# Performance work log

Measured on AMD Instinct MI355X. Metric: run time of the kernel, lower is better.

The kernel has to match this reference:

```python
import jax, jax.numpy as jnp
import numpy as np

N_NODES = 100000
T = 1024        # number of visits / hyperedges (GRU sequence length)
IN = 128        # in_channel
HID = 256       # hid_channel


def setup_inputs() -> dict:
    key = jax.random.key(0)
    ks = jax.random.split(key, 7)
    X = jax.random.normal(ks[0], (N_NODES, IN), dtype=jnp.float32)
    H = jax.random.uniform(ks[1], (N_NODES, T), dtype=jnp.float32)
    s = 1.0 / np.sqrt(HID)  # torch default GRU init scale
    w_ih = jax.random.uniform(ks[2], (3 * HID, IN), jnp.float32, -s, s)
    w_hh = jax.random.uniform(ks[3], (3 * HID, HID), jnp.float32, -s, s)
    b_ih = jax.random.uniform(ks[4], (3 * HID,), jnp.float32, -s, s)
    b_hh = jax.random.uniform(ks[5], (3 * HID,), jnp.float32, -s, s)
    w_attn = jax.random.uniform(ks[6], (HID,), jnp.float32, -s, s)
    return {"X": X, "H": H, "w_ih": w_ih, "w_hh": w_hh,
            "b_ih": b_ih, "b_hh": b_hh, "w_attn": w_attn}


def _gru(visit_emb, w_ih, w_hh, b_ih, b_hh):
    # Precompute input-side gates for all timesteps: [T, 3H]
    gx = visit_emb @ w_ih.T + b_ih

    def step(h, gx_t):
        gh = h @ w_hh.T + b_hh
        xr, xz, xn = jnp.split(gx_t, 3)
        hr, hz, hn = jnp.split(gh, 3)
        r = jax.nn.sigmoid(xr + hr)
        z = jax.nn.sigmoid(xz + hz)
        n = jnp.tanh(xn + r * hn)
        h_new = (1.0 - z) * n + z * h
        return h_new, h_new

    h0 = jnp.zeros((HID,), visit_emb.dtype)
    _, hs = jax.lax.scan(step, h0, gx)
    return hs  # [T, HID]


def reference(X, H, w_ih, w_hh, b_ih, b_hh, w_attn):
    # visit_emb = H.T @ X : [T, IN]
    visit_emb = H.T @ X
    hs = _gru(visit_emb, w_ih, w_hh, b_ih, b_hh)          # [T, HID]
    alpha = jax.nn.softmax(hs @ w_attn)                    # [T]
    # sum(diag(alpha) @ hs, 0) == alpha-weighted sum of hidden states
    return alpha @ hs                                      # [HID]
```

## Files before the change

### kernel.cpp

```cpp
#include <hip/hip_runtime.h>
#include <hip/hip_fp16.h>

typedef _Float16 half8 __attribute__((ext_vector_type(8)));
typedef _Float16 half2v __attribute__((ext_vector_type(2)));
typedef float f32x4 __attribute__((ext_vector_type(4)));

#define T_STEPS 1024
#define INC 128
#define HIDC 256
#define G3 768
#define NN 100000
#define KSPLIT 32
#define NCHUNK 3125
#define XS_STRIDE 144

__device__ __forceinline__ float dpp_xor1(float v){
  int t = __builtin_amdgcn_update_dpp(0, __float_as_int(v), 0xB1, 0xF, 0xF, true);
  return __int_as_float(t);
}

__global__ __launch_bounds__(512) void k_phase1(const float* __restrict__ X,
                                                const float* __restrict__ Hm,
                                                float* __restrict__ part){
  const int bid = blockIdx.x;
  const int xcd = bid & 7;
  const int idx = bid >> 3;
  const int ks  = xcd * 4 + (idx & 3);
  const int tt  = idx >> 2;
  const int t0 = tt * 128;
  const int nbeg = ks * NCHUNK;
  const int nend = nbeg + NCHUNK;
  __shared__ float Hs[16][128];
  __shared__ float Xs[16 * XS_STRIDE];
  const int tid = threadIdx.x;
  const int tx = tid & 15;
  const int ty = tid >> 4;
  const int sr = tid >> 5;
  const int sc = tid & 31;
  const int xskew = tx * 8 + (tx >> 2) * 4;

  float acc[4][8];
  #pragma unroll
  for (int r = 0; r < 4; r++)
    #pragma unroll
    for (int q = 0; q < 8; q++) acc[r][q] = 0.f;

  float4 hv = make_float4(0.f,0.f,0.f,0.f), xv = make_float4(0.f,0.f,0.f,0.f);
  {
    int n = nbeg + sr;
    if (n < nend){
      hv = *(const float4*)(Hm + (size_t)n * T_STEPS + t0 + sc * 4);
      xv = *(const float4*)(X  + (size_t)n * INC + sc * 4);
    }
  }

  for (int n0 = nbeg; n0 < nend; n0 += 16){
    __builtin_amdgcn_s_barrier();
    asm volatile("" ::: "memory");
    *(float4*)&Hs[sr][sc * 4] = hv;
    {
      int g = sc >> 1, hf = sc & 1;
      *(float4*)&Xs[sr * XS_STRIDE + g * 8 + (g >> 2) * 4 + hf * 4] = xv;
    }
    asm volatile("s_waitcnt lgkmcnt(0)" ::: "memory");
    __builtin_amdgcn_s_barrier();
    asm volatile("" ::: "memory");

    {
      int nn = n0 + 16 + sr;
      hv = make_float4(0.f,0.f,0.f,0.f);
      xv = make_float4(0.f,0.f,0.f,0.f);
      if (nn < nend){
        hv = *(const float4*)(Hm + (size_t)nn * T_STEPS + t0 + sc * 4);
        xv = *(const float4*)(X  + (size_t)nn * INC + sc * 4);
      }
    }

    #pragma unroll
    for (int i = 0; i < 16; i++){
      float4 h4 = *(const float4*)&Hs[i][ty * 4];
      float4 x0 = *(const float4*)&Xs[i * XS_STRIDE + xskew];
      float4 x1 = *(const float4*)&Xs[i * XS_STRIDE + xskew + 4];
      float xr[8] = {x0.x,x0.y,x0.z,x0.w,x1.x,x1.y,x1.z,x1.w};
      float hr[4] = {h4.x,h4.y,h4.z,h4.w};
      #pragma unroll
      for (int r = 0; r < 4; r++)
        #pragma unroll
        for (int q = 0; q < 8; q++)
          acc[r][q] += hr[r] * xr[q];
    }
  }
  #pragma unroll
  for (int r = 0; r < 4; r++){
    size_t o = ((size_t)ks * T_STEPS + t0 + ty * 4 + r) * INC + tx * 8;
    *(float4*)&part[o]     = make_float4(acc[r][0], acc[r][1], acc[r][2], acc[r][3]);
    *(float4*)&part[o + 4] = make_float4(acc[r][4], acc[r][5], acc[r][6], acc[r][7]);
  }
}

__global__ __launch_bounds__(256) void k_reduce(const float* __restrict__ part,
                                                float* __restrict__ ve){
  int idx = blockIdx.x * 256 + threadIdx.x;
  float s = 0.f;
  #pragma unroll
  for (int ks = 0; ks < KSPLIT; ks++) s += part[(size_t)ks * (T_STEPS * INC) + idx];
  ve[idx] = s;
}

__global__ __launch_bounds__(768) void k_gx(const float* __restrict__ ve,
                                            const float* __restrict__ w_ih,
                                            const float* __restrict__ b_ih,
                                            const float* __restrict__ b_hh,
                                            float* __restrict__ gxq){
  const int t = blockIdx.x;
  const int j = threadIdx.x;
  __shared__ float4 v4[32];
  if (j < 32) v4[j] = *(const float4*)(ve + (size_t)t * INC + j * 4);
  __syncthreads();
  const float4* wr = (const float4*)(w_ih + (size_t)j * INC);
  float a0 = 0.f, a1 = 0.f, a2 = 0.f, a3 = 0.f;
  #pragma unroll
  for (int q = 0; q < 32; q++){
    float4 w = wr[q]; float4 v = v4[q];
    a0 += w.x * v.x; a1 += w.y * v.y; a2 += w.z * v.z; a3 += w.w * v.w;
  }
  float bias = b_ih[j] + (j < 512 ? b_hh[j] : 0.f);
  gxq[(size_t)t * 1024 + (j & 255) * 4 + (j >> 8)] = (a0 + a1) + (a2 + a3) + bias;
}

__global__ __launch_bounds__(512, 2) void k_gru(const float* __restrict__ w_hh,
                                                const float* __restrict__ b_hh,
                                                const float* __restrict__ gxq,
                                                float* __restrict__ hs){
  const int tid  = threadIdx.x;
  const int unit = tid >> 1;
  const int ks   = tid & 1;
  const int k0   = ks * 128;

  __shared__ _Float16 hbuf[2][256];

  half2v Bp[3][64];
  #pragma unroll
  for (int g = 0; g < 3; g++){
    const float* wr = w_hh + (size_t)(g * 256 + unit) * HIDC + k0;
    #pragma unroll
    for (int c = 0; c < 32; c++){
      float4 v = *(const float4*)(wr + c * 4);
      half2v p0; p0[0] = (_Float16)v.x; p0[1] = (_Float16)v.y;
      half2v p1; p1[0] = (_Float16)v.z; p1[1] = (_Float16)v.w;
      Bp[g][2 * c]     = p0;
      Bp[g][2 * c + 1] = p1;
    }
  }
  const float bn = b_hh[512 + unit];
  float hprev = 0.f;
  if (tid < 256) hbuf[0][tid] = (_Float16)0.f;
  __syncthreads();

  f32x4 gq = *(const f32x4*)(gxq + (size_t)unit * 4);

  for (int t = 0; t < T_STEPS; t++){
    const _Float16* hb = &hbuf[t & 1][k0];
    float ar0 = 0.f, ar1 = 0.f, az0 = 0.f, az1 = 0.f, an0 = 0.f, an1 = 0.f;
    #pragma unroll
    for (int c = 0; c < 16; c++){
      half8 hv = *(const half8*)(hb + c * 8);
      #pragma unroll
      for (int q = 0; q < 4; q++){
        half2v hp; hp[0] = hv[2 * q]; hp[1] = hv[2 * q + 1];
        if (c & 1){
          ar1 = __builtin_amdgcn_fdot2(hp, Bp[0][4 * c + q], ar1, false);
          az1 = __builtin_amdgcn_fdot2(hp, Bp[1][4 * c + q], az1, false);
          an1 = __builtin_amdgcn_fdot2(hp, Bp[2][4 * c + q], an1, false);
        } else {
          ar0 = __builtin_amdgcn_fdot2(hp, Bp[0][4 * c + q], ar0, false);
          az0 = __builtin_amdgcn_fdot2(hp, Bp[1][4 * c + q], az0, false);
          an0 = __builtin_amdgcn_fdot2(hp, Bp[2][4 * c + q], an0, false);
        }
      }
    }
    f32x4 gq_n = *(const f32x4*)(gxq + (size_t)(t + 1) * 1024 + unit * 4);

    float dr = ar0 + ar1; dr += dpp_xor1(dr);
    float dz = az0 + az1; dz += dpp_xor1(dz);
    float dn = an0 + an1; dn += dpp_xor1(dn);

    float r = 1.f / (1.f + __expf(-(gq[0] + dr)));
    float z = 1.f / (1.f + __expf(-(gq[1] + dz)));
    float pre = gq[2] + r * (dn + bn);
    float ax = fabsf(pre);
    float e = __expf(-2.f * ax);
    float th = (1.f - e) / (1.f + e);
    float n = copysignf(th, pre);
    float hnew = n + z * (hprev - n);
    hprev = hnew;
    if (ks == 0){
      hbuf[(t + 1) & 1][unit] = (_Float16)hnew;
      hs[(size_t)t * HIDC + unit] = hnew;
    }
    gq = gq_n;
    __syncthreads();
  }
}

__global__ __launch_bounds__(64) void k_logits(const float* __restrict__ hs,
                                               const float* __restrict__ w_attn,
                                               float* __restrict__ logits){
  int t = blockIdx.x;
  int l = threadIdx.x;
  float4 hv = *(const float4*)(hs + (size_t)t * HIDC + l * 4);
  float4 wv = *(const float4*)(w_attn + l * 4);
  float p = hv.x * wv.x + hv.y * wv.y + hv.z * wv.z + hv.w * wv.w;
  #pragma unroll
  for (int o = 32; o > 0; o >>= 1) p += __shfl_down(p, o);
  if (l == 0) logits[t] = p;
}

__global__ __launch_bounds__(1024) void k_attn(const float* __restrict__ logits,
                                               const float* __restrict__ hs,
                                               float* __restrict__ out){
  __shared__ float sm[1024];
  __shared__ float al[1024];
  __shared__ float ps[4][HIDC];
  int tid = threadIdx.x;
  float lg = logits[tid];
  sm[tid] = lg; __syncthreads();
  for (int s = 512; s > 0; s >>= 1){
    if (tid < s) sm[tid] = fmaxf(sm[tid], sm[tid + s]);
    __syncthreads();
  }
  float mx = sm[0]; __syncthreads();
  float e = __expf(lg - mx);
  sm[tid] = e; __syncthreads();
  for (int s = 512; s > 0; s >>= 1){
    if (tid < s) sm[tid] += sm[tid + s];
    __syncthreads();
  }
  float inv = 1.f / sm[0];
  al[tid] = e * inv;
  __syncthreads();
  int c = tid & 255; int tq = tid >> 8;
  float acc = 0.f;
  for (int t = tq; t < T_STEPS; t += 4) acc += al[t] * hs[(size_t)t * HIDC + c];
  ps[tq][c] = acc; __syncthreads();
  if (tid < HIDC) out[tid] = (ps[0][tid] + ps[1][tid]) + (ps[2][tid] + ps[3][tid]);
}

extern "C" void kernel_launch(void* const* d_in, const int* in_sizes, int n_in,
                              void* d_out, int out_size, void* d_ws, size_t ws_size,
                              hipStream_t stream){
  const float* X      = (const float*)d_in[0];
  const float* Hm     = (const float*)d_in[1];
  const float* w_ih   = (const float*)d_in[2];
  const float* w_hh   = (const float*)d_in[3];
  const float* b_ih   = (const float*)d_in[4];
  const float* b_hh   = (const float*)d_in[5];
  const float* w_attn = (const float*)d_in[6];
  float* out = (float*)d_out;

  float* ws     = (float*)d_ws;
  float* part   = ws;
  float* ve     = part + 4194304;
  float* gxq    = ve + 131072;
  float* hs     = gxq + 1049600;
  float* logits = hs + 262144;

  k_phase1<<<256, 512, 0, stream>>>(X, Hm, part);
  k_reduce<<<512, 256, 0, stream>>>(part, ve);
  k_gx<<<1024, 768, 0, stream>>>(ve, w_ih, b_ih, b_hh, gxq);
  k_gru<<<1, 512, 0, stream>>>(w_hh, b_hh, gxq, hs);
  k_logits<<<1024, 64, 0, stream>>>(hs, w_attn, logits);
  k_attn<<<1, 1024, 0, stream>>>(logits, hs, out);
}
```

Before: 2.196 ms.

## Split GRU recurrent matvec four ways per unit across 1024 threads

```diff
diff --git a/kernel.cpp b/kernel.cpp
--- a/kernel.cpp
+++ b/kernel.cpp
@@ -16,6 +16,10 @@
 
 __device__ __forceinline__ float dpp_xor1(float v){
   int t = __builtin_amdgcn_update_dpp(0, __float_as_int(v), 0xB1, 0xF, 0xF, true);
+  return __int_as_float(t);
+}
+__device__ __forceinline__ float dpp_xor2(float v){
+  int t = __builtin_amdgcn_update_dpp(0, __float_as_int(v), 0x4E, 0xF, 0xF, true);
   return __int_as_float(t);
 }
 
@@ -128,23 +132,23 @@
   gxq[(size_t)t * 1024 + (j & 255) * 4 + (j >> 8)] = (a0 + a1) + (a2 + a3) + bias;
 }
 
-__global__ __launch_bounds__(512, 2) void k_gru(const float* __restrict__ w_hh,
-                                                const float* __restrict__ b_hh,
-                                                const float* __restrict__ gxq,
-                                                float* __restrict__ hs){
+__global__ __launch_bounds__(1024) void k_gru(const float* __restrict__ w_hh,
+                                              const float* __restrict__ b_hh,
+                                              const float* __restrict__ gxq,
+                                              float* __restrict__ hs){
   const int tid  = threadIdx.x;
-  const int unit = tid >> 1;
-  const int ks   = tid & 1;
-  const int k0   = ks * 128;
+  const int unit = tid >> 2;
+  const int ks   = tid & 3;
+  const int k0   = ks * 64;
 
   __shared__ _Float16 hbuf[2][256];
 
-  half2v Bp[3][64];
+  half2v Bp[3][32];
   #pragma unroll
   for (int g = 0; g < 3; g++){
     const float* wr = w_hh + (size_t)(g * 256 + unit) * HIDC + k0;
     #pragma unroll
-    for (int c = 0; c < 32; c++){
+    for (int c = 0; c < 16; c++){
       float4 v = *(const float4*)(wr + c * 4);
       half2v p0; p0[0] = (_Float16)v.x; p0[1] = (_Float16)v.y;
       half2v p1; p1[0] = (_Float16)v.z; p1[1] = (_Float16)v.w;
@@ -157,33 +161,34 @@
   if (tid < 256) hbuf[0][tid] = (_Float16)0.f;
   __syncthreads();
 
-  f32x4 gq = *(const f32x4*)(gxq + (size_t)unit * 4);
-
   for (int t = 0; t < T_STEPS; t++){
     const _Float16* hb = &hbuf[t & 1][k0];
+    f32x4 gq = *(const f32x4*)(gxq + (size_t)t * 1024 + unit * 4);
+
     float ar0 = 0.f, ar1 = 0.f, az0 = 0.f, az1 = 0.f, an0 = 0.f, an1 = 0.f;
     #pragma unroll
-    for (int c = 0; c < 16; c++){
-      half8 hv = *(const half8*)(hb + c * 8);
+    for (int c = 0; c < 8; c++){
+      const int cc = (c + 2 * ks) & 7;
+      half8 hv = *(const half8*)(hb + cc * 8);
       #pragma unroll
       for (int q = 0; q < 4; q++){
         half2v hp; hp[0] = hv[2 * q]; hp[1] = hv[2 * q + 1];
+        const int j = cc * 4 + q;
         if (c & 1){
-          ar1 = __builtin_amdgcn_fdot2(hp, Bp[0][4 * c + q], ar1, false);
-          az1 = __builtin_amdgcn_fdot2(hp, Bp[1][4 * c + q], az1, false);
-          an1 = __builtin_amdgcn_fdot2(hp, Bp[2][4 * c + q], an1, false);
+          ar1 = __builtin_amdgcn_fdot2(hp, Bp[0][j], ar1, false);
+          az1 = __builtin_amdgcn_fdot2(hp, Bp[1][j], az1, false);
+          an1 = __builtin_amdgcn_fdot2(hp, Bp[2][j], an1, false);
         } else {
-          ar0 = __builtin_amdgcn_fdot2(hp, Bp[0][4 * c + q], ar0, false);
-          az0 = __builtin_amdgcn_fdot2(hp, Bp[1][4 * c + q], az0, false);
-          an0 = __builtin_amdgcn_fdot2(hp, Bp[2][4 * c + q], an0, false);
+          ar0 = __builtin_amdgcn_fdot2(hp, Bp[0][j], ar0, false);
+          az0 = __builtin_amdgcn_fdot2(hp, Bp[1][j], az0, false);
+          an0 = __builtin_amdgcn_fdot2(hp, Bp[2][j], an0, false);
         }
       }
     }
-    f32x4 gq_n = *(const f32x4*)(gxq + (size_t)(t + 1) * 1024 + unit * 4);
-
-    float dr = ar0 + ar1; dr += dpp_xor1(dr);
-    float dz = az0 + az1; dz += dpp_xor1(dz);
-    float dn = an0 + an1; dn += dpp_xor1(dn);
+
+    float dr = ar0 + ar1; dr += dpp_xor1(dr); dr += dpp_xor2(dr);
+    float dz = az0 + az1; dz += dpp_xor1(dz); dz += dpp_xor2(dz);
+    float dn = an0 + an1; dn += dpp_xor1(dn); dn += dpp_xor2(dn);
 
     float r = 1.f / (1.f + __expf(-(gq[0] + dr)));
     float z = 1.f / (1.f + __expf(-(gq[1] + dz)));
@@ -198,8 +203,9 @@
       hbuf[(t + 1) & 1][unit] = (_Float16)hnew;
       hs[(size_t)t * HIDC + unit] = hnew;
     }
-    gq = gq_n;
-    __syncthreads();
+    asm volatile("s_waitcnt lgkmcnt(0)" ::: "memory");
+    __builtin_amdgcn_s_barrier();
+    asm volatile("" ::: "memory");
   }
 }
 
@@ -268,7 +274,7 @@
   k_phase1<<<256, 512, 0, stream>>>(X, Hm, part);
   k_reduce<<<512, 256, 0, stream>>>(part, ve);
   k_gx<<<1024, 768, 0, stream>>>(ve, w_ih, b_ih, b_hh, gxq);
-  k_gru<<<1, 512, 0, stream>>>(w_hh, b_hh, gxq, hs);
+  k_gru<<<1, 1024, 0, stream>>>(w_hh, b_hh, gxq, hs);
   k_logits<<<1024, 64, 0, stream>>>(hs, w_attn, logits);
   k_attn<<<1, 1024, 0, stream>>>(logits, hs, out);
 }
```

Measured after the change: 2.667 ms. 21.5% more time.
